# Performance work log

Hardware: AMD Instinct MI355X
Metric: run time of the kernel (lower is better)

The kernel has to match this reference:

```python
import jax, jax.numpy as jnp
import numpy as np

B, H, S, D = 8, 8, 1024, 64

def setup_inputs() -> dict:
    key = jax.random.key(0)
    kq, kk, kv = jax.random.split(key, 3)
    queries = jax.random.normal(kq, (B, H, S, D), dtype=jnp.float32)
    keys = jax.random.normal(kk, (B, H, S, D), dtype=jnp.float32)
    values = jax.random.normal(kv, (B, H, S, D), dtype=jnp.float32)
    return {"queries": queries, "keys": keys, "values": values}

def reference(queries, keys, values):
    # scale = 1/sqrt(D) since self.scale is None
    scale = 1.0 / jnp.sqrt(jnp.asarray(queries.shape[-1], queries.dtype))
    # scores: [B, H, S, S]
    scores = jnp.einsum("bhqd,bhkd->bhqk", queries, keys) * scale
    # mask_flag=False -> no masking; dropout treated as identity (eval mode)
    attn = jax.nn.softmax(scores, axis=-1)
    output = jnp.einsum("bhqk,bhkd->bhqd", attn, values)
    return (output, attn)
```

## Files before the change

kernel.cpp:

```cpp
#include <hip/hip_runtime.h>
#include <hip/hip_bf16.h>

#define B_ 8
#define H_ 8
#define S_ 1024
#define D_ 64

typedef __attribute__((ext_vector_type(8))) short bf16x8;
typedef __attribute__((ext_vector_type(4))) float f32x4;

__device__ __forceinline__ short f2bf(float f) {
  union { float f; unsigned u; } x; x.f = f;
  unsigned r = (x.u + 0x7FFFu + ((x.u >> 16) & 1u)) >> 16;
  return (short)r;
}

__device__ __forceinline__ bf16x8 load8_bf(const float* p) {
  float4 a = *(const float4*)p;
  float4 b = *(const float4*)(p + 4);
  bf16x8 f;
  f[0] = f2bf(a.x); f[1] = f2bf(a.y); f[2] = f2bf(a.z); f[3] = f2bf(a.w);
  f[4] = f2bf(b.x); f[5] = f2bf(b.y); f[6] = f2bf(b.z); f[7] = f2bf(b.w);
  return f;
}

constexpr int QT  = 16;
constexpr int NW  = 4;
constexpr int TPW = (S_ / 16) / NW;
constexpr int PPAD = 8;

__global__ __launch_bounds__(256) void attn_fused(
    const float* __restrict__ Q, const float* __restrict__ K,
    const float* __restrict__ V, float* __restrict__ O,
    float* __restrict__ A)
{
  const int bh   = blockIdx.y;
  const int q0   = blockIdx.x * QT;
  const int tid  = threadIdx.x;
  const int wave = tid >> 6;
  const int lane = tid & 63;
  const int m    = lane & 15;
  const int quad = lane >> 4;

  const float* Qb = Q + (size_t)bh * S_ * D_;
  const float* Kb = K + (size_t)bh * S_ * D_;
  const float* Vb = V + (size_t)bh * S_ * D_;
  float* Ob = O + (size_t)bh * S_ * D_;
  float* Ab = A + (size_t)bh * S_ * S_;

  __shared__ float redmax[NW][QT];
  __shared__ float redsum[NW][QT];
  __shared__ short pbuf[QT][S_ + PPAD];

  bf16x8 qf0, qf1;
  {
    const float* qp = Qb + (size_t)(q0 + m) * D_ + quad * 8;
    qf0 = load8_bf(qp);
    qf1 = load8_bf(qp + 32);
  }

  f32x4 acc[TPW];
  #pragma unroll
  for (int t = 0; t < TPW; ++t) {
    const int kt = t * NW + wave;
    const float* kp = Kb + (size_t)(kt * 16 + m) * D_ + quad * 8;
    bf16x8 kf0 = load8_bf(kp);
    bf16x8 kf1 = load8_bf(kp + 32);
    f32x4 c = {0.f, 0.f, 0.f, 0.f};
    c = __builtin_amdgcn_mfma_f32_16x16x32_bf16(qf0, kf0, c, 0, 0, 0);
    c = __builtin_amdgcn_mfma_f32_16x16x32_bf16(qf1, kf1, c, 0, 0, 0);
    acc[t] = c * 0.125f;
  }

  float tmp4[4];
  #pragma unroll
  for (int r = 0; r < 4; ++r) {
    float v = acc[0][r];
    #pragma unroll
    for (int t = 1; t < TPW; ++t) v = fmaxf(v, acc[t][r]);
    v = fmaxf(v, __shfl_xor(v, 1));
    v = fmaxf(v, __shfl_xor(v, 2));
    v = fmaxf(v, __shfl_xor(v, 4));
    v = fmaxf(v, __shfl_xor(v, 8));
    tmp4[r] = v;
  }
  if (m == 0) {
    #pragma unroll
    for (int r = 0; r < 4; ++r) redmax[wave][quad * 4 + r] = tmp4[r];
  }
  __syncthreads();

  #pragma unroll
  for (int r = 0; r < 4; ++r) {
    const int row = quad * 4 + r;
    const float gm = fmaxf(fmaxf(redmax[0][row], redmax[1][row]),
                           fmaxf(redmax[2][row], redmax[3][row]));
    float s = 0.f;
    #pragma unroll
    for (int t = 0; t < TPW; ++t) {
      float p = __builtin_exp2f((acc[t][r] - gm) * 1.4426950408889634f);
      acc[t][r] = p;
      s += p;
    }
    s += __shfl_xor(s, 1);
    s += __shfl_xor(s, 2);
    s += __shfl_xor(s, 4);
    s += __shfl_xor(s, 8);
    tmp4[r] = s;
  }
  if (m == 0) {
    #pragma unroll
    for (int r = 0; r < 4; ++r) redsum[wave][quad * 4 + r] = tmp4[r];
  }
  __syncthreads();

  float rinv[4];
  #pragma unroll
  for (int r = 0; r < 4; ++r) {
    const int row = quad * 4 + r;
    const float tot = (redsum[0][row] + redsum[1][row]) +
                      (redsum[2][row] + redsum[3][row]);
    rinv[r] = 1.f / tot;
  }

  #pragma unroll
  for (int t = 0; t < TPW; ++t) {
    const int kt = t * NW + wave;
    #pragma unroll
    for (int r = 0; r < 4; ++r) {
      const int row = quad * 4 + r;
      const float p = acc[t][r] * rinv[r];
      Ab[(size_t)(q0 + row) * S_ + kt * 16 + m] = p;
      pbuf[row][kt * 16 + m] = f2bf(p);
    }
  }
  __syncthreads();

  f32x4 oc = {0.f, 0.f, 0.f, 0.f};
  const int n0 = wave * 16;
  for (int kc = 0; kc < S_ / 32; ++kc) {
    bf16x8 af = *(const bf16x8*)&pbuf[m][kc * 32 + quad * 8];
    const float* vp = Vb + (size_t)(kc * 32 + quad * 8) * D_ + n0 + m;
    bf16x8 bv;
    #pragma unroll
    for (int j = 0; j < 8; ++j) bv[j] = f2bf(vp[(size_t)j * D_]);
    oc = __builtin_amdgcn_mfma_f32_16x16x32_bf16(af, bv, oc, 0, 0, 0);
  }
  #pragma unroll
  for (int r = 0; r < 4; ++r) {
    Ob[(size_t)(q0 + quad * 4 + r) * D_ + n0 + m] = oc[r];
  }
}

extern "C" void kernel_launch(void* const* d_in, const int* in_sizes, int n_in,
                              void* d_out, int out_size, void* d_ws, size_t ws_size,
                              hipStream_t stream) {
  const float* Q = (const float*)d_in[0];
  const float* K = (const float*)d_in[1];
  const float* V = (const float*)d_in[2];
  float* O = (float*)d_out;
  float* A = O + (size_t)B_ * H_ * S_ * D_;
  dim3 grid(S_ / QT, B_ * H_);
  attn_fused<<<grid, NW * 64, 0, stream>>>(Q, K, V, O, A);
}
```

Before: 494.2 us.

## Pre-convert Q/K to bf16 and pre-transpose V into workspace before attention

Adds pre-pass kernels that convert Q and K to bf16 and convert V to a transposed bf16 layout in workspace. The main kernel then reads half-size contiguous vectors instead of re-converting fp32 data in every block, and V reads become contiguous instead of strided scalar gathers. It also uses nontemporal stores for the large attention matrix and splits the PV accumulation into two independent chains. The cost is three extra launches and extra workspace traffic.

```diff
diff --git a/kernel.cpp b/kernel.cpp
--- a/kernel.cpp
+++ b/kernel.cpp
@@ -15,13 +15,47 @@
   return (short)r;
 }
 
-__device__ __forceinline__ bf16x8 load8_bf(const float* p) {
-  float4 a = *(const float4*)p;
-  float4 b = *(const float4*)(p + 4);
+__global__ __launch_bounds__(256) void cvt_bf16(const float* __restrict__ in,
+                                                short* __restrict__ out) {
+  const size_t i = ((size_t)blockIdx.x * 256 + threadIdx.x) * 8;
+  float4 a = *(const float4*)(in + i);
+  float4 b = *(const float4*)(in + i + 4);
   bf16x8 f;
   f[0] = f2bf(a.x); f[1] = f2bf(a.y); f[2] = f2bf(a.z); f[3] = f2bf(a.w);
   f[4] = f2bf(b.x); f[5] = f2bf(b.y); f[6] = f2bf(b.z); f[7] = f2bf(b.w);
-  return f;
+  *(bf16x8*)(out + i) = f;
+}
+
+__global__ __launch_bounds__(256) void vtrans(const float* __restrict__ V,
+                                              short* __restrict__ Vt) {
+  const int bh = blockIdx.y;
+  const int s0 = blockIdx.x * 64;
+  __shared__ float tile[64][65];
+  const float* Vb = V + ((size_t)bh * S_ + s0) * D_;
+  const int t = threadIdx.x;
+  {
+    const int rbase = t >> 4;
+    const int c4 = (t & 15) * 4;
+    #pragma unroll
+    for (int i = 0; i < 4; ++i) {
+      const int row = i * 16 + rbase;
+      float4 v = *(const float4*)(Vb + (size_t)row * D_ + c4);
+      tile[row][c4 + 0] = v.x; tile[row][c4 + 1] = v.y;
+      tile[row][c4 + 2] = v.z; tile[row][c4 + 3] = v.w;
+    }
+  }
+  __syncthreads();
+  const int d = t >> 2;
+  const int sq = (t & 3) * 16;
+  short* op = Vt + ((size_t)bh * D_ + d) * S_ + s0 + sq;
+  bf16x8 a, b;
+  #pragma unroll
+  for (int j = 0; j < 8; ++j) {
+    a[j] = f2bf(tile[sq + j][d]);
+    b[j] = f2bf(tile[sq + 8 + j][d]);
+  }
+  *(bf16x8*)op = a;
+  *(bf16x8*)(op + 8) = b;
 }
 
 constexpr int QT  = 16;
@@ -30,9 +64,9 @@
 constexpr int PPAD = 8;
 
 __global__ __launch_bounds__(256) void attn_fused(
-    const float* __restrict__ Q, const float* __restrict__ K,
-    const float* __restrict__ V, float* __restrict__ O,
-    float* __restrict__ A)
+    const short* __restrict__ Qb16, const short* __restrict__ Kb16,
+    const short* __restrict__ Vt, const float* __restrict__ V_unused,
+    float* __restrict__ O, float* __restrict__ A)
 {
   const int bh   = blockIdx.y;
   const int q0   = blockIdx.x * QT;
@@ -42,9 +76,9 @@
   const int m    = lane & 15;
   const int quad = lane >> 4;
 
-  const float* Qb = Q + (size_t)bh * S_ * D_;
-  const float* Kb = K + (size_t)bh * S_ * D_;
-  const float* Vb = V + (size_t)bh * S_ * D_;
+  const short* Qb  = Qb16 + (size_t)bh * S_ * D_;
+  const short* Kb  = Kb16 + (size_t)bh * S_ * D_;
+  const short* Vtb = Vt   + (size_t)bh * D_ * S_;
   float* Ob = O + (size_t)bh * S_ * D_;
   float* Ab = A + (size_t)bh * S_ * S_;
 
@@ -54,18 +88,18 @@
 
   bf16x8 qf0, qf1;
   {
-    const float* qp = Qb + (size_t)(q0 + m) * D_ + quad * 8;
-    qf0 = load8_bf(qp);
-    qf1 = load8_bf(qp + 32);
+    const short* qp = Qb + (size_t)(q0 + m) * D_ + quad * 8;
+    qf0 = *(const bf16x8*)qp;
+    qf1 = *(const bf16x8*)(qp + 32);
   }
 
   f32x4 acc[TPW];
   #pragma unroll
   for (int t = 0; t < TPW; ++t) {
     const int kt = t * NW + wave;
-    const float* kp = Kb + (size_t)(kt * 16 + m) * D_ + quad * 8;
-    bf16x8 kf0 = load8_bf(kp);
-    bf16x8 kf1 = load8_bf(kp + 32);
+    const short* kp = Kb + (size_t)(kt * 16 + m) * D_ + quad * 8;
+    bf16x8 kf0 = *(const bf16x8*)kp;
+    bf16x8 kf1 = *(const bf16x8*)(kp + 32);
     f32x4 c = {0.f, 0.f, 0.f, 0.f};
     c = __builtin_amdgcn_mfma_f32_16x16x32_bf16(qf0, kf0, c, 0, 0, 0);
     c = __builtin_amdgcn_mfma_f32_16x16x32_bf16(qf1, kf1, c, 0, 0, 0);
@@ -118,9 +152,8 @@
   #pragma unroll
   for (int r = 0; r < 4; ++r) {
     const int row = quad * 4 + r;
-    const float tot = (redsum[0][row] + redsum[1][row]) +
-                      (redsum[2][row] + redsum[3][row]);
-    rinv[r] = 1.f / tot;
+    rinv[r] = 1.f / ((redsum[0][row] + redsum[1][row]) +
+                     (redsum[2][row] + redsum[3][row]));
   }
 
   #pragma unroll
@@ -130,25 +163,27 @@
     for (int r = 0; r < 4; ++r) {
       const int row = quad * 4 + r;
       const float p = acc[t][r] * rinv[r];
-      Ab[(size_t)(q0 + row) * S_ + kt * 16 + m] = p;
+      __builtin_nontemporal_store(p, &Ab[(size_t)(q0 + row) * S_ + kt * 16 + m]);
       pbuf[row][kt * 16 + m] = f2bf(p);
     }
   }
   __syncthreads();
 
-  f32x4 oc = {0.f, 0.f, 0.f, 0.f};
+  f32x4 oc0 = {0.f, 0.f, 0.f, 0.f};
+  f32x4 oc1 = {0.f, 0.f, 0.f, 0.f};
   const int n0 = wave * 16;
-  for (int kc = 0; kc < S_ / 32; ++kc) {
-    bf16x8 af = *(const bf16x8*)&pbuf[m][kc * 32 + quad * 8];
-    const float* vp = Vb + (size_t)(kc * 32 + quad * 8) * D_ + n0 + m;
-    bf16x8 bv;
-    #pragma unroll
-    for (int j = 0; j < 8; ++j) bv[j] = f2bf(vp[(size_t)j * D_]);
-    oc = __builtin_amdgcn_mfma_f32_16x16x32_bf16(af, bv, oc, 0, 0, 0);
-  }
-  #pragma unroll
-  for (int r = 0; r < 4; ++r) {
-    Ob[(size_t)(q0 + quad * 4 + r) * D_ + n0 + m] = oc[r];
+  const short* vrow = Vtb + (size_t)(n0 + m) * S_;
+  for (int kc = 0; kc < S_ / 32; kc += 2) {
+    bf16x8 af0 = *(const bf16x8*)&pbuf[m][kc * 32 + quad * 8];
+    bf16x8 bv0 = *(const bf16x8*)(vrow + kc * 32 + quad * 8);
+    oc0 = __builtin_amdgcn_mfma_f32_16x16x32_bf16(af0, bv0, oc0, 0, 0, 0);
+    bf16x8 af1 = *(const bf16x8*)&pbuf[m][(kc + 1) * 32 + quad * 8];
+    bf16x8 bv1 = *(const bf16x8*)(vrow + (kc + 1) * 32 + quad * 8);
+    oc1 = __builtin_amdgcn_mfma_f32_16x16x32_bf16(af1, bv1, oc1, 0, 0, 0);
+  }
+  #pragma unroll
+  for (int r = 0; r < 4; ++r) {
+    Ob[(size_t)(q0 + quad * 4 + r) * D_ + n0 + m] = oc0[r] + oc1[r];
   }
 }
 
@@ -160,6 +195,17 @@
   const float* V = (const float*)d_in[2];
   float* O = (float*)d_out;
   float* A = O + (size_t)B_ * H_ * S_ * D_;
+
+  const size_t NEL = (size_t)B_ * H_ * S_ * D_;
+  short* Qbf = (short*)d_ws;
+  short* Kbf = Qbf + NEL;
+  short* Vtb = Kbf + NEL;
+
+  const int cvt_blocks = (int)(NEL / 8 / 256);
+  cvt_bf16<<<cvt_blocks, 256, 0, stream>>>(Q, Qbf);
+  cvt_bf16<<<cvt_blocks, 256, 0, stream>>>(K, Kbf);
+  vtrans<<<dim3(S_ / 64, B_ * H_), 256, 0, stream>>>(V, Vtb);
+
   dim3 grid(S_ / QT, B_ * H_);
-  attn_fused<<<grid, NW * 64, 0, stream>>>(Q, K, V, O, A);
-}
+  attn_fused<<<grid, NW * 64, 0, stream>>>(Qbf, Kbf, Vtb, V, O, A);
+}
```

Measured after the change: 408.5 us. 1.21x faster.
